# Optimization experiments

Hardware: AMD Instinct MI355X
Metric: run time of the kernel (lower is better)

Reference implementation:

```python
import jax, jax.numpy as jnp
import numpy as np

EPS = 1e-5  # BatchNorm eps
K = 10      # knn neighbors

def mish(x):
    return x * jnp.tanh(jax.nn.softplus(x))

def block(h, w, g, b, m, v):
    # 1x1 conv (no bias) + BN (inference stats) + Mish; h: [..., Cin], w: [Cout, Cin]
    y = jnp.einsum('...c,oc->...o', h, w)
    y = (y - m) * (g * jax.lax.rsqrt(v + EPS)) + b
    return mish(y)

def graph_feature(xt, k):
    # xt: [B, N, C] -> edge features [B, N, k, 2C] = cat(neighbor - center, center)
    xx = jnp.sum(xt * xt, axis=-1)                       # [B,N]
    inner = jnp.einsum('bnc,bmc->bnm', xt, xt)           # [B,N,N]
    neg_dist = 2.0 * inner - xx[:, :, None] - xx[:, None, :]
    idx = jax.lax.top_k(neg_dist, k)[1]                  # [B,N,k] nearest (incl. self)
    feat = jax.vmap(lambda a, i: a[i])(xt, idx)          # [B,N,k,C]
    center = jnp.broadcast_to(xt[:, :, None, :], feat.shape)
    return jnp.concatenate([feat - center, center], axis=-1)

def _bn_params(key, c):
    k1, k2, k3, k4 = jax.random.split(key, 4)
    g = 1.0 + 0.1 * jax.random.normal(k1, (c,), jnp.float32)
    b = 0.1 * jax.random.normal(k2, (c,), jnp.float32)
    m = 0.1 * jax.random.normal(k3, (c,), jnp.float32)
    v = 0.5 + jax.random.uniform(k4, (c,), jnp.float32)
    return g, b, m, v

def setup_inputs() -> dict:
    key = jax.random.key(0)
    B, C, N = 4, 3, 4096
    emb = 1024
    ks = jax.random.split(key, 20)
    d = {'x': jax.random.normal(ks[0], (B, C, N), jnp.float32)}
    dims = {'1': (64, 2 * C), '2': (64, 64), '3': (64, 128), '4': (64, 64),
            '6': (emb, 128), '7': (512, emb + 128), '8': (256, 512)}
    i = 1
    for name, (co, ci) in dims.items():
        d['w' + name] = jax.random.normal(ks[i], (co, ci), jnp.float32) * (1.0 / np.sqrt(ci))
        g, b, m, v = _bn_params(ks[i + 1], co)
        d['g' + name], d['b' + name], d['m' + name], d['v' + name] = g, b, m, v
        i += 2
    d['w9'] = jax.random.normal(ks[i], (2, 256), jnp.float32) * (1.0 / np.sqrt(256))
    return d

def reference(x, w1, g1, b1, m1, v1, w2, g2, b2, m2, v2, w3, g3, b3, m3, v3,
              w4, g4, b4, m4, v4, w6, g6, b6, m6, v6, w7, g7, b7, m7, v7,
              w8, g8, b8, m8, v8, w9):
    B, C, N = x.shape
    xt = jnp.transpose(x, (0, 2, 1))                    # [B,N,3]
    ef = graph_feature(xt, K)                           # [B,N,k,6]
    h = block(block(ef, w1, g1, b1, m1, v1), w2, g2, b2, m2, v2)
    x1 = jnp.max(h, axis=2)                             # [B,N,64]
    ef = graph_feature(x1, K)                           # [B,N,k,128]
    h = block(block(ef, w3, g3, b3, m3, v3), w4, g4, b4, m4, v4)
    x2 = jnp.max(h, axis=2)                             # [B,N,64]
    cat = jnp.concatenate([x1, x2], axis=-1)            # [B,N,128]
    h6 = block(cat, w6, g6, b6, m6, v6)                 # [B,N,1024]
    gmax = jnp.max(h6, axis=1, keepdims=True)           # [B,1,1024]
    gb = jnp.broadcast_to(gmax, (B, N, gmax.shape[-1]))
    cat2 = jnp.concatenate([gb, x1, x2], axis=-1)       # [B,N,1152]
    h = block(block(cat2, w7, g7, b7, m7, v7), w8, g8, b8, m8, v8)
    out = jnp.einsum('bnc,oc->bon', h, w9)              # [B,2,N]
    return out
```

## Files before the change

### kernel.cpp

```cpp
#include <hip/hip_runtime.h>
#include <cfloat>


#define BN_EPS 1e-5f

__device__ __forceinline__ float mish_f(float x) {
  float e = __expf(x);
  float num = e * (e + 2.0f);
  float r = x * (num / (num + 2.0f));
  return (x > 44.0f) ? x : r;
}

__device__ __forceinline__ float rl_f(float v, int l) {
  return __uint_as_float((unsigned)__builtin_amdgcn_readlane((int)__float_as_uint(v), l));
}

__device__ __forceinline__ unsigned enc_f(float f) {
  unsigned b = __float_as_uint(f);
  return (b & 0x80000000u) ? ~b : (b | 0x80000000u);
}
__device__ __forceinline__ float dec_f(unsigned u) {
  unsigned b = (u & 0x80000000u) ? (u ^ 0x80000000u) : ~u;
  return __uint_as_float(b);
}

__device__ __forceinline__ void topk_insert(float (&v)[10], int (&id)[10], float nd, int m) {
  if (nd > v[9]) {
    v[9] = nd; id[9] = m;
#pragma unroll
    for (int j = 9; j > 0; --j) {
      if (v[j] > v[j - 1]) {
        float tv = v[j]; v[j] = v[j - 1]; v[j - 1] = tv;
        int ti = id[j]; id[j] = id[j - 1]; id[j - 1] = ti;
      }
    }
  }
}

__device__ __forceinline__ void topk_bl(float (&v)[10], int (&id)[10], float nd, int m) {
  bool c[10];
#pragma unroll
  for (int j = 0; j < 10; ++j) c[j] = nd > v[j];
#pragma unroll
  for (int j = 9; j >= 1; --j) {
    v[j]  = c[j - 1] ? v[j - 1]  : (c[j] ? nd : v[j]);
    id[j] = c[j - 1] ? id[j - 1] : (c[j] ? m  : id[j]);
  }
  v[0]  = c[0] ? nd : v[0];
  id[0] = c[0] ? m  : id[0];
}

__global__ __launch_bounds__(256) void knn1_k(const float* __restrict__ x, int* __restrict__ idx1) {
  __shared__ float pls[3][4100];
  const int tid = threadIdx.x;
  const int rowBase = blockIdx.x * 64;
  const int b = rowBase >> 12;
  const float* xb = x + (size_t)b * 3 * 4096;
#pragma unroll
  for (int c = 0; c < 3; ++c) {
#pragma unroll
    for (int s = 0; s < 16; ++s) {
      int li = tid + 256 * s;
      pls[c][(li >> 10) * 1025 + (li & 1023)] = xb[c * 4096 + li];
    }
  }
  __syncthreads();
  const int sub = tid & 3;
  const int nloc = (rowBase & 4095) + (tid >> 2);
  float pnx = xb[nloc], pny = xb[4096 + nloc], pnz = xb[8192 + nloc];
  float xxn = pnx * pnx; xxn = fmaf(pny, pny, xxn); xxn = fmaf(pnz, pnz, xxn);
  float v[10]; int id[10];
#pragma unroll
  for (int j = 0; j < 10; ++j) { v[j] = -FLT_MAX; id[j] = -1; }
  const int base = sub * 1025;
  for (int i = 0; i < 1024; ++i) {
    float mx = pls[0][base + i], my = pls[1][base + i], mz = pls[2][base + i];
    float in = mx * pnx; in = fmaf(my, pny, in); in = fmaf(mz, pnz, in);
    float xm = mx * mx;  xm = fmaf(my, my, xm);  xm = fmaf(mz, mz, xm);
    float nd = 2.0f * in - xxn - xm;
    topk_insert(v, id, nd, sub * 1024 + i);
  }
  int k0 = -1, k1 = -1, k2 = -1;
#pragma unroll
  for (int r = 0; r < 10; ++r) {
    float mv = v[0]; int mi = id[0];
    { float ov = __shfl_xor(mv, 1); int oi = __shfl_xor(mi, 1);
      if (ov > mv || (ov == mv && oi < mi)) { mv = ov; mi = oi; } }
    { float ov = __shfl_xor(mv, 2); int oi = __shfl_xor(mi, 2);
      if (ov > mv || (ov == mv && oi < mi)) { mv = ov; mi = oi; } }
    if (id[0] == mi) {
#pragma unroll
      for (int j = 0; j < 9; ++j) { v[j] = v[j + 1]; id[j] = id[j + 1]; }
      v[9] = -FLT_MAX; id[9] = -1;
    }
    if ((r & 3) == sub) { if (r < 4) k0 = mi; else if (r < 8) k1 = mi; else k2 = mi; }
  }
  const int obase = (rowBase + (tid >> 2)) * 10;
  if (sub == 0)      { idx1[obase + 0] = k0; idx1[obase + 4] = k1; idx1[obase + 8] = k2; }
  else if (sub == 1) { idx1[obase + 1] = k0; idx1[obase + 5] = k1; idx1[obase + 9] = k2; }
  else if (sub == 2) { idx1[obase + 2] = k0; idx1[obase + 6] = k1; }
  else               { idx1[obase + 3] = k0; idx1[obase + 7] = k1; }
}

__global__ __launch_bounds__(256) void pre1_k(const float* __restrict__ x, const float* __restrict__ w1,
                                              float* __restrict__ e1m, float* __restrict__ e1n) {
  int gt = blockIdx.x * 256 + threadIdx.x;
  int pt = gt >> 6, c = gt & 63;
  int b = pt >> 12, n = pt & 4095;
  const float* xb = x + (size_t)b * 3 * 4096;
  float px = xb[n], py = xb[4096 + n], pz = xb[8192 + n];
  const float* wr = w1 + c * 6;
  float a0 = wr[0], a1 = wr[1], a2 = wr[2], b0 = wr[3], b1 = wr[4], b2 = wr[5];
  float vm = a0 * px; vm = fmaf(a1, py, vm); vm = fmaf(a2, pz, vm);
  float un = (b0 - a0) * px; un = fmaf(b1 - a1, py, un); un = fmaf(b2 - a2, pz, un);
  e1m[(size_t)pt * 64 + c] = vm;
  e1n[(size_t)pt * 64 + c] = un;
}

template <bool WRITE_XX>
__global__ __launch_bounds__(256) void edge_k(
    const int* __restrict__ idx,
    const float* __restrict__ vm, const float* __restrict__ un, int stride,
    const float* __restrict__ w,
    const float* __restrict__ ga, const float* __restrict__ ba, const float* __restrict__ ma, const float* __restrict__ va,
    const float* __restrict__ gb, const float* __restrict__ bb, const float* __restrict__ mb, const float* __restrict__ vb,
    float* __restrict__ outCat, int outOff, float* __restrict__ xxOut) {
  const int tid = threadIdx.x;
  const int wid = tid >> 6, lane = tid & 63;
  const int r = blockIdx.x * 4 + wid;
  const int mbase = (r >> 12) << 12;
  float4 wv[16];
  const float4* wp = (const float4*)(w + lane * 64);
#pragma unroll
  for (int i = 0; i < 16; ++i) wv[i] = wp[i];
  float s1 = ga[lane] * rsqrtf(va[lane] + BN_EPS); float t1 = ba[lane] - ma[lane] * s1;
  float s2 = gb[lane] * rsqrtf(vb[lane] + BN_EPS); float t2 = bb[lane] - mb[lane] * s2;
  float uc = un[(size_t)r * stride + lane];
  float best = -FLT_MAX;
#pragma unroll
  for (int kk = 0; kk < 10; ++kk) {
    int m = idx[r * 10 + kk];
    float pre = vm[(size_t)(mbase + m) * stride + lane] + uc;
    float h1 = mish_f(fmaf(pre, s1, t1));
    float acc = 0.f;
#pragma unroll
    for (int j4 = 0; j4 < 16; ++j4) {
      float4 wq = wv[j4];
      acc = fmaf(wq.x, rl_f(h1, 4 * j4 + 0), acc);
      acc = fmaf(wq.y, rl_f(h1, 4 * j4 + 1), acc);
      acc = fmaf(wq.z, rl_f(h1, 4 * j4 + 2), acc);
      acc = fmaf(wq.w, rl_f(h1, 4 * j4 + 3), acc);
    }
    float h2 = mish_f(fmaf(acc, s2, t2));
    best = fmaxf(best, h2);
  }
  outCat[(size_t)r * 128 + outOff + lane] = best;
  if (WRITE_XX) {
    float q = best * best;
#pragma unroll
    for (int o = 1; o < 64; o <<= 1) q += __shfl_xor(q, o);
    if (lane == 0) xxOut[r] = q;
  }
}

#define KNN2_CHUNKS 8
__global__ __launch_bounds__(256)
__attribute__((amdgpu_waves_per_eu(2, 2)))
void knn2_k(const float* __restrict__ cat,
            const float* __restrict__ xx2,
            float* __restrict__ pv, int* __restrict__ pi) {
  __shared__ float tile[128 * 68];
  __shared__ float xxm[128];
  const int tid = threadIdx.x;
  const int r = blockIdx.x * 256 + tid;
  const int nbase = (r >> 12) << 12;
  const int cb = blockIdx.y * 512;

  float4 q[16];
  const float4* qp = (const float4*)(cat + (size_t)r * 128);
#pragma unroll
  for (int s = 0; s < 16; ++s) q[s] = qp[s];
#pragma unroll
  for (int s = 0; s < 16; ++s)
    asm volatile("" : "+v"(q[s].x), "+v"(q[s].y), "+v"(q[s].z), "+v"(q[s].w));

  float v[10]; int id[10];
#pragma unroll
  for (int j = 0; j < 10; ++j) { v[j] = -FLT_MAX; id[j] = -1; }

  for (int t = 0; t < 4; ++t) {
    __syncthreads();
#pragma unroll
    for (int s = 0; s < 8; ++s) {
      int g = tid + 256 * s;
      int cand = g >> 4, c4 = g & 15;
      float4 val = *(const float4*)(cat + (size_t)(nbase + cb + t * 128 + cand) * 128 + c4 * 4);
      *(float4*)(tile + cand * 68 + c4 * 4) = val;
    }
    if (tid < 128) xxm[tid] = xx2[nbase + cb + t * 128 + tid];
    __syncthreads();
#pragma unroll 1
    for (int m = 0; m < 128; ++m) {
      const float4* crow = (const float4*)(tile + m * 68);
      float a0 = 0.f, a1 = 0.f, a2 = 0.f, a3 = 0.f;
#pragma unroll
      for (int c4 = 0; c4 < 16; c4 += 4) {
        float4 t0 = crow[c4 + 0], t1 = crow[c4 + 1], t2 = crow[c4 + 2], t3 = crow[c4 + 3];
        a0 = fmaf(t0.x, q[c4 + 0].x, a0); a0 = fmaf(t0.y, q[c4 + 0].y, a0);
        a0 = fmaf(t0.z, q[c4 + 0].z, a0); a0 = fmaf(t0.w, q[c4 + 0].w, a0);
        a1 = fmaf(t1.x, q[c4 + 1].x, a1); a1 = fmaf(t1.y, q[c4 + 1].y, a1);
        a1 = fmaf(t1.z, q[c4 + 1].z, a1); a1 = fmaf(t1.w, q[c4 + 1].w, a1);
        a2 = fmaf(t2.x, q[c4 + 2].x, a2); a2 = fmaf(t2.y, q[c4 + 2].y, a2);
        a2 = fmaf(t2.z, q[c4 + 2].z, a2); a2 = fmaf(t2.w, q[c4 + 2].w, a2);
        a3 = fmaf(t3.x, q[c4 + 3].x, a3); a3 = fmaf(t3.y, q[c4 + 3].y, a3);
        a3 = fmaf(t3.z, q[c4 + 3].z, a3); a3 = fmaf(t3.w, q[c4 + 3].w, a3);
      }
      float nd = 2.0f * ((a0 + a1) + (a2 + a3)) - xxm[m];
      topk_bl(v, id, nd, cb + t * 128 + m);
    }
  }
  const size_t ob = ((size_t)blockIdx.y * 16384 + r) * 10;
#pragma unroll
  for (int j = 0; j < 10; ++j) { pv[ob + j] = v[j]; pi[ob + j] = id[j]; }
}

__global__ __launch_bounds__(256) void knn2m_k(const float* __restrict__ pv,
                                               const int* __restrict__ pi,
                                               int* __restrict__ idx2) {
  const int r = blockIdx.x * 256 + threadIdx.x;
  float v[10]; int id[10];
#pragma unroll
  for (int j = 0; j < 10; ++j) { v[j] = -FLT_MAX; id[j] = -1; }
  for (int c = 0; c < KNN2_CHUNKS; ++c) {
    const size_t base = ((size_t)c * 16384 + r) * 10;
    if (pv[base] > v[9]) {
#pragma unroll
      for (int j = 0; j < 10; ++j) topk_insert(v, id, pv[base + j], pi[base + j]);
    }
  }
#pragma unroll
  for (int j = 0; j < 10; ++j) idx2[r * 10 + j] = id[j];
}

__global__ void w3s_k(const float* __restrict__ w3, float* __restrict__ w3s) {
  int t = blockIdx.x * 256 + threadIdx.x;
  int c = t >> 6, k = t & 63;
  float v;
  if (c < 64) v = w3[c * 128 + k];
  else { int cc = c - 64; v = w3[cc * 128 + 64 + k] - w3[cc * 128 + k]; }
  w3s[t] = v;
}

template <int QM, int QN, int EPI>
__global__ __launch_bounds__(256) void gemm_k(
    const float* __restrict__ A, int lda,
    const float* __restrict__ W, int ldw,
    float* __restrict__ C, int ldc, int K, int Ntot,
    const float* __restrict__ eg, const float* __restrict__ eb,
    const float* __restrict__ em, const float* __restrict__ ev,
    const float* __restrict__ pbBias, unsigned int* __restrict__ gmaxOut) {
  constexpr int BM = 64 * QM, BN = 64 * QN;
  __shared__ float aL[16][BM];
  __shared__ float bL[16][BN];
  __shared__ unsigned int cm[BN];
  const int tid = threadIdx.x;
  const int tm = tid >> 4, tn = tid & 15;
  const int rowBase = blockIdx.x * BM;
  const int colBase = blockIdx.y * BN;
  float acc[QM][QN][4][4] = {};
  if (EPI == 2 && tid < BN) cm[tid] = 0u;
  const int nkt = K >> 4;
  for (int kt = 0; kt < nkt; ++kt) {
#pragma unroll
    for (int s = 0; s < QM; ++s) {
      int fi = tid + 256 * s;
      int m = fi >> 2, k4 = fi & 3;
      float4 t4 = *(const float4*)(A + (size_t)(rowBase + m) * lda + (kt << 4) + k4 * 4);
      aL[k4 * 4 + 0][m] = t4.x; aL[k4 * 4 + 1][m] = t4.y;
      aL[k4 * 4 + 2][m] = t4.z; aL[k4 * 4 + 3][m] = t4.w;
    }
#pragma unroll
    for (int s = 0; s < QN; ++s) {
      int fi = tid + 256 * s;
      int n = fi >> 2, k4 = fi & 3;
      float4 t4 = *(const float4*)(W + (size_t)(colBase + n) * ldw + (kt << 4) + k4 * 4);
      bL[k4 * 4 + 0][n] = t4.x; bL[k4 * 4 + 1][n] = t4.y;
      bL[k4 * 4 + 2][n] = t4.z; bL[k4 * 4 + 3][n] = t4.w;
    }
    __syncthreads();
#pragma unroll
    for (int k = 0; k < 16; ++k) {
      float ar[QM][4], br[QN][4];
#pragma unroll
      for (int q = 0; q < QM; ++q) {
        float4 t4 = *(const float4*)&aL[k][q * 64 + tm * 4];
        ar[q][0] = t4.x; ar[q][1] = t4.y; ar[q][2] = t4.z; ar[q][3] = t4.w;
      }
#pragma unroll
      for (int q = 0; q < QN; ++q) {
        float4 t4 = *(const float4*)&bL[k][q * 64 + tn * 4];
        br[q][0] = t4.x; br[q][1] = t4.y; br[q][2] = t4.z; br[q][3] = t4.w;
      }
#pragma unroll
      for (int qm = 0; qm < QM; ++qm)
#pragma unroll
        for (int qn = 0; qn < QN; ++qn)
#pragma unroll
          for (int i = 0; i < 4; ++i)
#pragma unroll
            for (int j = 0; j < 4; ++j)
              acc[qm][qn][i][j] = fmaf(ar[qm][i], br[qn][j], acc[qm][qn][i][j]);
    }
    __syncthreads();
  }
  if (EPI == 0) {
#pragma unroll
    for (int qm = 0; qm < QM; ++qm)
#pragma unroll
      for (int i = 0; i < 4; ++i) {
        int row = rowBase + qm * 64 + tm * 4 + i;
#pragma unroll
        for (int qn = 0; qn < QN; ++qn) {
          float4 o;
          o.x = acc[qm][qn][i][0]; o.y = acc[qm][qn][i][1];
          o.z = acc[qm][qn][i][2]; o.w = acc[qm][qn][i][3];
          *(float4*)(C + (size_t)row * ldc + colBase + qn * 64 + tn * 4) = o;
        }
      }
  } else {
    const int bidx = rowBase >> 12;
    float sc[QN][4], sh[QN][4];
#pragma unroll
    for (int qn = 0; qn < QN; ++qn)
#pragma unroll
      for (int j = 0; j < 4; ++j) {
        int cg = colBase + qn * 64 + tn * 4 + j;
        float s = eg[cg] * rsqrtf(ev[cg] + BN_EPS);
        sc[qn][j] = s;
        sh[qn][j] = (EPI == 3) ? pbBias[bidx * Ntot + cg] : (eb[cg] - em[cg] * s);
      }
    if (EPI == 2) {
      float cmax[QN][4];
#pragma unroll
      for (int qn = 0; qn < QN; ++qn)
#pragma unroll
        for (int j = 0; j < 4; ++j) cmax[qn][j] = -FLT_MAX;
#pragma unroll
      for (int qm = 0; qm < QM; ++qm)
#pragma unroll
        for (int qn = 0; qn < QN; ++qn)
#pragma unroll
          for (int i = 0; i < 4; ++i)
#pragma unroll
            for (int j = 0; j < 4; ++j) {
              float vv = mish_f(fmaf(acc[qm][qn][i][j], sc[qn][j], sh[qn][j]));
              cmax[qn][j] = fmaxf(cmax[qn][j], vv);
            }
#pragma unroll
      for (int qn = 0; qn < QN; ++qn)
#pragma unroll
        for (int j = 0; j < 4; ++j)
          atomicMax(&cm[qn * 64 + tn * 4 + j], enc_f(cmax[qn][j]));
      __syncthreads();
      if (tid < BN) atomicMax(&gmaxOut[bidx * Ntot + colBase + tid], cm[tid]);
    } else {
#pragma unroll
      for (int qm = 0; qm < QM; ++qm)
#pragma unroll
        for (int i = 0; i < 4; ++i) {
          int row = rowBase + qm * 64 + tm * 4 + i;
#pragma unroll
          for (int qn = 0; qn < QN; ++qn) {
            float4 o;
            o.x = mish_f(fmaf(acc[qm][qn][i][0], sc[qn][0], sh[qn][0]));
            o.y = mish_f(fmaf(acc[qm][qn][i][1], sc[qn][1], sh[qn][1]));
            o.z = mish_f(fmaf(acc[qm][qn][i][2], sc[qn][2], sh[qn][2]));
            o.w = mish_f(fmaf(acc[qm][qn][i][3], sc[qn][3], sh[qn][3]));
            *(float4*)(C + (size_t)row * ldc + colBase + qn * 64 + tn * 4) = o;
          }
        }
    }
  }
}

__global__ __launch_bounds__(256) void bias7_k(const unsigned int* __restrict__ gmaxU,
                                               const float* __restrict__ w7,
                                               const float* __restrict__ g7, const float* __restrict__ b7,
                                               const float* __restrict__ m7, const float* __restrict__ v7,
                                               float* __restrict__ bias7) {
  __shared__ float gl[1024];
  const int tid = threadIdx.x;
  const int batch = blockIdx.x >> 1, half = blockIdx.x & 1;
#pragma unroll
  for (int s = 0; s < 4; ++s) gl[tid + 256 * s] = dec_f(gmaxU[batch * 1024 + tid + 256 * s]);
  __syncthreads();
  const int ch = half * 256 + tid;
  const float4* wr = (const float4*)(w7 + (size_t)ch * 1152);
  float acc = 0.f;
  for (int j4 = 0; j4 < 256; ++j4) {
    float4 w = wr[j4];
    float4 g = *(const float4*)&gl[j4 * 4];
    acc = fmaf(w.x, g.x, acc); acc = fmaf(w.y, g.y, acc);
    acc = fmaf(w.z, g.z, acc); acc = fmaf(w.w, g.w, acc);
  }
  float s7 = g7[ch] * rsqrtf(v7[ch] + BN_EPS);
  bias7[batch * 512 + ch] = acc * s7 + (b7[ch] - m7[ch] * s7);
}

__global__ __launch_bounds__(256) void out_k(const float* __restrict__ h8,
                                             const float* __restrict__ w9, float* __restrict__ out) {
  __shared__ float w9l[512];
  const int tid = threadIdx.x;
  w9l[tid] = w9[tid];
  w9l[256 + tid] = w9[256 + tid];
  __syncthreads();
  const int t = blockIdx.x * 256 + tid;
  const int b = t >> 12, n = t & 4095;
  const float4* hr = (const float4*)(h8 + (size_t)t * 256);
  float a0 = 0.f, a1 = 0.f;
#pragma unroll
  for (int j4 = 0; j4 < 64; ++j4) {
    float4 h = hr[j4];
    float4 wa = *(const float4*)&w9l[j4 * 4];
    float4 wb = *(const float4*)&w9l[256 + j4 * 4];
    a0 = fmaf(h.x, wa.x, a0); a0 = fmaf(h.y, wa.y, a0);
    a0 = fmaf(h.z, wa.z, a0); a0 = fmaf(h.w, wa.w, a0);
    a1 = fmaf(h.x, wb.x, a1); a1 = fmaf(h.y, wb.y, a1);
    a1 = fmaf(h.z, wb.z, a1); a1 = fmaf(h.w, wb.w, a1);
  }
  out[(size_t)b * 8192 + n] = a0;
  out[(size_t)b * 8192 + 4096 + n] = a1;
}

extern "C" void kernel_launch(void* const* d_in, const int* in_sizes, int n_in,
                              void* d_out, int out_size, void* d_ws, size_t ws_size,
                              hipStream_t stream) {
  const float* x  = (const float*)d_in[0];
  const float* w1 = (const float*)d_in[1];
  const float* g1 = (const float*)d_in[2];
  const float* b1 = (const float*)d_in[3];
  const float* m1 = (const float*)d_in[4];
  const float* v1 = (const float*)d_in[5];
  const float* w2 = (const float*)d_in[6];
  const float* g2 = (const float*)d_in[7];
  const float* b2 = (const float*)d_in[8];
  const float* m2 = (const float*)d_in[9];
  const float* v2 = (const float*)d_in[10];
  const float* w3 = (const float*)d_in[11];
  const float* g3 = (const float*)d_in[12];
  const float* b3 = (const float*)d_in[13];
  const float* m3 = (const float*)d_in[14];
  const float* v3 = (const float*)d_in[15];
  const float* w4 = (const float*)d_in[16];
  const float* g4 = (const float*)d_in[17];
  const float* b4 = (const float*)d_in[18];
  const float* m4 = (const float*)d_in[19];
  const float* v4 = (const float*)d_in[20];
  const float* w6 = (const float*)d_in[21];
  const float* g6 = (const float*)d_in[22];
  const float* b6 = (const float*)d_in[23];
  const float* m6 = (const float*)d_in[24];
  const float* v6 = (const float*)d_in[25];
  const float* w7 = (const float*)d_in[26];
  const float* g7 = (const float*)d_in[27];
  const float* b7 = (const float*)d_in[28];
  const float* m7 = (const float*)d_in[29];
  const float* v7 = (const float*)d_in[30];
  const float* w8 = (const float*)d_in[31];
  const float* g8 = (const float*)d_in[32];
  const float* b8 = (const float*)d_in[33];
  const float* m8 = (const float*)d_in[34];
  const float* v8 = (const float*)d_in[35];
  const float* w9 = (const float*)d_in[36];

  float* ws = (float*)d_ws;
  int* idx1       = (int*)(ws + 0);
  int* idx2       = (int*)(ws + 163840);
  float* xx2      = ws + 327680;
  unsigned* gmax  = (unsigned*)(ws + 344064);
  float* bias7    = ws + 348160;
  float* w3s      = ws + 350208;
  float* e1n      = ws + 358400;
  float* e1m      = ws + 1406976;
  float* pre3     = ws + 358400;
  float* cat      = ws + 2455552;
  float* h7       = ws + 4552704;
  float* h8       = ws + 12941312;
  float* knn2pv   = h7;
  int*   knn2pi   = (int*)(h7 + 1310720);

  hipMemsetAsync(gmax, 0, 4096 * sizeof(unsigned), stream);

  knn1_k<<<256, 256, 0, stream>>>(x, idx1);
  pre1_k<<<4096, 256, 0, stream>>>(x, w1, e1m, e1n);
  edge_k<true><<<4096, 256, 0, stream>>>(idx1, e1m, e1n, 64, w2,
                                         g1, b1, m1, v1, g2, b2, m2, v2,
                                         cat, 0, xx2);
  w3s_k<<<32, 256, 0, stream>>>(w3, w3s);
  gemm_k<1, 2, 0><<<dim3(256, 1), 256, 0, stream>>>(cat, 128, w3s, 64, pre3, 128, 64, 0,
                                                    nullptr, nullptr, nullptr, nullptr, nullptr, nullptr);
  knn2_k<<<dim3(64, KNN2_CHUNKS), 256, 0, stream>>>(cat, xx2, knn2pv, knn2pi);
  knn2m_k<<<64, 256, 0, stream>>>(knn2pv, knn2pi, idx2);
  edge_k<false><<<4096, 256, 0, stream>>>(idx2, pre3, pre3 + 64, 128, w4,
                                          g3, b3, m3, v3, g4, b4, m4, v4,
                                          cat, 64, nullptr);
  gemm_k<2, 2, 2><<<dim3(128, 8), 256, 0, stream>>>(cat, 128, w6, 128, nullptr, 0, 128, 1024,
                                                    g6, b6, m6, v6, nullptr, gmax);
  bias7_k<<<8, 256, 0, stream>>>(gmax, w7, g7, b7, m7, v7, bias7);
  gemm_k<2, 2, 3><<<dim3(128, 4), 256, 0, stream>>>(cat, 128, w7 + 1024, 1152, h7, 512, 128, 512,
                                                    g7, nullptr, nullptr, v7, bias7, nullptr);
  gemm_k<1, 2, 1><<<dim3(256, 2), 256, 0, stream>>>(h7, 512, w8, 512, h8, 256, 512, 256,
                                                    g8, b8, m8, v8, nullptr, nullptr);
  out_k<<<64, 256, 0, stream>>>(h8, w9, (float*)d_out);
}
```

Before: 1.142 ms.

## Split knn2 into tiled distance GEMM plus separate streaming top-k pass

When the workspace is large enough, the second kNN is split in two. A register-tiled 128x128 GEMM first writes the full per-batch inner-product matrix (4x4096x4096 floats, about 256 MB) to global memory. A separate kernel then streams columns of that matrix and runs the per-row top-k insertion. The aim is to replace the fused knn2 kernel's per-thread dot products from LDS with a higher-reuse GEMM, at the cost of a large extra global write and read. If the workspace is too small, the old fused kernel runs instead.

```diff
diff --git a/kernel.cpp b/kernel.cpp
--- a/kernel.cpp
+++ b/kernel.cpp
@@ -163,7 +163,97 @@
   }
 }
 
+__global__ __launch_bounds__(256) void dist_k(const float* __restrict__ cat, float* __restrict__ D) {
+  __shared__ float aL[16][128];
+  __shared__ float bL[16][128];
+  const int tid = threadIdx.x;
+  const int tm = tid >> 4, tn = tid & 15;
+  const int rowBase = blockIdx.x * 128;
+  const int colBase = blockIdx.y * 128;
+  const float* Wb = cat + (size_t)((rowBase >> 12) << 12) * 128;
+  float acc[2][2][4][4] = {};
+  for (int kt = 0; kt < 4; ++kt) {
+#pragma unroll
+    for (int s = 0; s < 2; ++s) {
+      int fi = tid + 256 * s;
+      int m = fi >> 2, k4 = fi & 3;
+      float4 t4 = *(const float4*)(cat + (size_t)(rowBase + m) * 128 + (kt << 4) + k4 * 4);
+      aL[k4 * 4 + 0][m] = t4.x; aL[k4 * 4 + 1][m] = t4.y;
+      aL[k4 * 4 + 2][m] = t4.z; aL[k4 * 4 + 3][m] = t4.w;
+    }
+#pragma unroll
+    for (int s = 0; s < 2; ++s) {
+      int fi = tid + 256 * s;
+      int n = fi >> 2, k4 = fi & 3;
+      float4 t4 = *(const float4*)(Wb + (size_t)(colBase + n) * 128 + (kt << 4) + k4 * 4);
+      bL[k4 * 4 + 0][n] = t4.x; bL[k4 * 4 + 1][n] = t4.y;
+      bL[k4 * 4 + 2][n] = t4.z; bL[k4 * 4 + 3][n] = t4.w;
+    }
+    __syncthreads();
+#pragma unroll
+    for (int k = 0; k < 16; ++k) {
+      float ar[2][4], br[2][4];
+#pragma unroll
+      for (int q = 0; q < 2; ++q) {
+        float4 t4 = *(const float4*)&aL[k][q * 64 + tm * 4];
+        ar[q][0] = t4.x; ar[q][1] = t4.y; ar[q][2] = t4.z; ar[q][3] = t4.w;
+      }
+#pragma unroll
+      for (int q = 0; q < 2; ++q) {
+        float4 t4 = *(const float4*)&bL[k][q * 64 + tn * 4];
+        br[q][0] = t4.x; br[q][1] = t4.y; br[q][2] = t4.z; br[q][3] = t4.w;
+      }
+#pragma unroll
+      for (int qm = 0; qm < 2; ++qm)
+#pragma unroll
+        for (int qn = 0; qn < 2; ++qn)
+#pragma unroll
+          for (int i = 0; i < 4; ++i)
+#pragma unroll
+            for (int j = 0; j < 4; ++j)
+              acc[qm][qn][i][j] = fmaf(ar[qm][i], br[qn][j], acc[qm][qn][i][j]);
+    }
+    __syncthreads();
+  }
+#pragma unroll
+  for (int qm = 0; qm < 2; ++qm)
+#pragma unroll
+    for (int i = 0; i < 4; ++i) {
+      int row = rowBase + qm * 64 + tm * 4 + i;
+#pragma unroll
+      for (int qn = 0; qn < 2; ++qn) {
+        float4 o;
+        o.x = acc[qm][qn][i][0]; o.y = acc[qm][qn][i][1];
+        o.z = acc[qm][qn][i][2]; o.w = acc[qm][qn][i][3];
+        *(float4*)(D + (size_t)row * 4096 + colBase + qn * 64 + tn * 4) = o;
+      }
+    }
+}
+
 #define KNN2_CHUNKS 8
+__global__ __launch_bounds__(256) void topk_k(const float* __restrict__ D,
+                                              const float* __restrict__ xx2,
+                                              float* __restrict__ pv, int* __restrict__ pi) {
+  const int tid = threadIdx.x;
+  const int r = blockIdx.x * 256 + tid;
+  const int b = r >> 12, rl = r & 4095;
+  const int cb = blockIdx.y * 512;
+  const float* __restrict__ Dp = D + ((size_t)(b << 12) + cb) * 4096 + rl;
+  const float* __restrict__ xxp = xx2 + (b << 12) + cb;
+  float v[10]; int id[10];
+#pragma unroll
+  for (int j = 0; j < 10; ++j) { v[j] = -FLT_MAX; id[j] = -1; }
+#pragma unroll 1
+  for (int i = 0; i < 512; ++i) {
+    float inner = Dp[(size_t)i * 4096];
+    float nd = fmaf(2.0f, inner, -xxp[i]);
+    topk_bl(v, id, nd, cb + i);
+  }
+  const size_t ob = ((size_t)blockIdx.y * 16384 + r) * 10;
+#pragma unroll
+  for (int j = 0; j < 10; ++j) { pv[ob + j] = v[j]; pi[ob + j] = id[j]; }
+}
+
 __global__ __launch_bounds__(256)
 __attribute__((amdgpu_waves_per_eu(2, 2)))
 void knn2_k(const float* __restrict__ cat,
@@ -175,7 +265,6 @@
   const int r = blockIdx.x * 256 + tid;
   const int nbase = (r >> 12) << 12;
   const int cb = blockIdx.y * 512;
-
   float4 q[16];
   const float4* qp = (const float4*)(cat + (size_t)r * 128);
 #pragma unroll
@@ -183,11 +272,9 @@
 #pragma unroll
   for (int s = 0; s < 16; ++s)
     asm volatile("" : "+v"(q[s].x), "+v"(q[s].y), "+v"(q[s].z), "+v"(q[s].w));
-
   float v[10]; int id[10];
 #pragma unroll
   for (int j = 0; j < 10; ++j) { v[j] = -FLT_MAX; id[j] = -1; }
-
   for (int t = 0; t < 4; ++t) {
     __syncthreads();
 #pragma unroll
@@ -486,8 +573,11 @@
   float* cat      = ws + 2455552;
   float* h7       = ws + 4552704;
   float* h8       = ws + 12941312;
+  float* D        = ws + 17135616;
   float* knn2pv   = h7;
   int*   knn2pi   = (int*)(h7 + 1310720);
+
+  const bool bigD = ws_size >= (size_t)(17135616 + 67108864) * 4;
 
   hipMemsetAsync(gmax, 0, 4096 * sizeof(unsigned), stream);
 
@@ -499,7 +589,12 @@
   w3s_k<<<32, 256, 0, stream>>>(w3, w3s);
   gemm_k<1, 2, 0><<<dim3(256, 1), 256, 0, stream>>>(cat, 128, w3s, 64, pre3, 128, 64, 0,
                                                     nullptr, nullptr, nullptr, nullptr, nullptr, nullptr);
-  knn2_k<<<dim3(64, KNN2_CHUNKS), 256, 0, stream>>>(cat, xx2, knn2pv, knn2pi);
+  if (bigD) {
+    dist_k<<<dim3(128, 32), 256, 0, stream>>>(cat, D);
+    topk_k<<<dim3(64, KNN2_CHUNKS), 256, 0, stream>>>(D, xx2, knn2pv, knn2pi);
+  } else {
+    knn2_k<<<dim3(64, KNN2_CHUNKS), 256, 0, stream>>>(cat, xx2, knn2pv, knn2pi);
+  }
   knn2m_k<<<64, 256, 0, stream>>>(knn2pv, knn2pi, idx2);
   edge_k<false><<<4096, 256, 0, stream>>>(idx2, pre3, pre3 + 64, 128, w4,
                                           g3, b3, m3, v3, g4, b4, m4, v4,
```

New measurement: 1.148 ms. About the same (+0.5%).
